# Kernel optimization log

Hardware: AMD Instinct MI355X
Metric: run time of the kernel (lower is better)

The kernel has to match this reference:

```python
import jax, jax.numpy as jnp
import numpy as np

TAU_MEM = 0.02
THRESHOLD = 0.5
RESET_POTENTIAL = 0.0
SURROGATE_BETA = 4.0
LN_EPS = 1e-6

B, T, F_IN, F_OUT = 64, 1024, 512, 512


def fast_sigmoid(x, beta):
    # Continuous fast-sigmoid surrogate spike: 0.5 * (beta*x / (1 + beta*|x|)) + 0.5
    bx = beta * x
    return 0.5 * bx / (1.0 + jnp.abs(bx)) + 0.5


def setup_inputs() -> dict:
    key = jax.random.key(0)
    k1, k2, k3 = jax.random.split(key, 3)
    spikes = jax.random.uniform(k1, (B, T, F_IN), dtype=jnp.float32)
    W = jax.random.normal(k2, (F_IN, F_OUT), dtype=jnp.float32) / np.sqrt(F_IN)
    b = jnp.zeros((F_OUT,), dtype=jnp.float32)
    ln_scale = jnp.ones((F_OUT,), dtype=jnp.float32)
    ln_bias = jnp.zeros((F_OUT,), dtype=jnp.float32)
    return {"spikes": spikes, "W": W, "b": b, "ln_scale": ln_scale, "ln_bias": ln_bias}


def reference(spikes, W, b, ln_scale, ln_bias):
    # Dense projection of input spike trains: [B,T,F_in] -> [B,T,F_out]
    currents = jnp.einsum('bti,io->bto', spikes, W) + b

    alpha = jnp.exp(jnp.float32(-1.0 / TAU_MEM))

    def lif_step(v_mem, cur):
        v_mem = alpha * v_mem + (1.0 - alpha) * cur
        spike = fast_sigmoid(v_mem - THRESHOLD, SURROGATE_BETA)
        v_mem = v_mem * (1.0 - spike) + RESET_POTENTIAL * spike
        return v_mem, spike

    v0 = jnp.zeros((spikes.shape[0], W.shape[1]), dtype=currents.dtype)
    _, out = jax.lax.scan(lif_step, v0, jnp.transpose(currents, (1, 0, 2)))  # [T,B,F]
    out = jnp.transpose(out, (1, 0, 2))  # [B,T,F]

    # LayerNorm over last axis (flax defaults: eps=1e-6, scale & bias)
    mean = jnp.mean(out, axis=-1, keepdims=True)
    var = jnp.var(out, axis=-1, keepdims=True)
    out = (out - mean) * jax.lax.rsqrt(var + LN_EPS) * ln_scale + ln_bias
    return out
```

## Files before the change

### kernel.cpp

```cpp
#include <hip/hip_runtime.h>

#define THREADS 512
#define NBLK 1024

typedef _Float16 half8 __attribute__((ext_vector_type(8)));
typedef float floatx4 __attribute__((ext_vector_type(4)));

__global__ void wcvt_kernel(const float* __restrict__ W, unsigned short* __restrict__ Wt) {
  __shared__ float tile[32][33];
  const int tx = threadIdx.x, ty = threadIdx.y;
  const int nb = blockIdx.x * 32, kb = blockIdx.y * 32;
#pragma unroll
  for (int i = 0; i < 4; ++i)
    tile[ty + 8 * i][tx] = W[(size_t)(kb + ty + 8 * i) * 512 + nb + tx];
  __syncthreads();
#pragma unroll
  for (int i = 0; i < 4; ++i) {
    union { _Float16 h; unsigned short u; } v;
    v.h = (_Float16)tile[tx][ty + 8 * i];
    Wt[(size_t)(nb + ty + 8 * i) * 512 + kb + tx] = v.u;
  }
}

#define BBASE 16384

__global__ __launch_bounds__(THREADS, 4) void lif_fused_kernel(
    const float* __restrict__ A, const unsigned short* __restrict__ Wt,
    const float* __restrict__ bias, const float* __restrict__ lnw,
    const float* __restrict__ lnb, float* __restrict__ out) {
  __shared__ uint4 smem4[5120];
  unsigned char* smem = (unsigned char*)smem4;

  const int tid  = threadIdx.x;
  const int lane = tid & 63;
  const int wave = tid >> 6;
  const int wrow = wave >> 2;
  const int wcol = wave & 3;
  const int l15  = lane & 15;
  const int g    = lane >> 4;
  const int rowBase = blockIdx.x * 64;

  const int arow  = wave * 4 + (lane >> 4);
  const int aslot = (lane & 15) ^ (arow & 15);
  const float* asrcA = A + (size_t)(rowBase + arow) * 512 + aslot * 4;
  const unsigned short* bsrcB =
      Wt + (size_t)(wave * 8 + (lane >> 3)) * 512 + ((lane & 7) ^ (lane >> 3)) * 8;

  auto stage = [&](int c) {
#pragma unroll
    for (int j = 0; j < 2; ++j) {
      int off = j * 8192 + wave * 1024;
      off = __builtin_amdgcn_readfirstlane(off);
      __builtin_amdgcn_global_load_lds(
          (const __attribute__((address_space(1))) void*)(asrcA + (size_t)j * 16384 + c * 64),
          (__attribute__((address_space(3))) void*)(smem + off), 16, 0, 0);
    }
#pragma unroll
    for (int i = 0; i < 8; ++i) {
      int off = BBASE + i * 8192 + wave * 1024;
      off = __builtin_amdgcn_readfirstlane(off);
      __builtin_amdgcn_global_load_lds(
          (const __attribute__((address_space(1))) void*)(bsrcB + (size_t)i * 32768 + c * 64),
          (__attribute__((address_space(3))) void*)(smem + off), 16, 0, 0);
    }
  };

  const int aRowB = (wrow * 32 + l15) * 256;
  const int e0 = (g * 2) ^ l15;
  const unsigned char* aP00 = smem + aRowB + e0 * 16;
  const unsigned char* aP01 = smem + aRowB + (e0 ^ 1) * 16;
  const unsigned char* aP10 = smem + aRowB + (e0 ^ 8) * 16;
  const unsigned char* aP11 = smem + aRowB + (e0 ^ 9) * 16;
  const int bRowB = BBASE + (wcol * 128 + l15) * 128;
  const int f0 = g ^ (l15 & 7);
  const unsigned char* bP0 = smem + bRowB + f0 * 16;
  const unsigned char* bP1 = smem + bRowB + (f0 ^ 4) * 16;

  floatx4 acc[2][8];
#pragma unroll
  for (int m = 0; m < 2; ++m)
#pragma unroll
    for (int n = 0; n < 8; ++n)
      acc[m][n] = (floatx4){0.f, 0.f, 0.f, 0.f};

  auto mk = [](float4 lo, float4 hi) {
    half8 t;
    t[0] = (_Float16)lo.x; t[1] = (_Float16)lo.y;
    t[2] = (_Float16)lo.z; t[3] = (_Float16)lo.w;
    t[4] = (_Float16)hi.x; t[5] = (_Float16)hi.y;
    t[6] = (_Float16)hi.z; t[7] = (_Float16)hi.w;
    return t;
  };

  auto compute = [&]() {
    {
      half8 a0 = mk(*(const float4*)aP00, *(const float4*)aP01);
      half8 a1 = mk(*(const float4*)(aP00 + 4096), *(const float4*)(aP01 + 4096));
      __builtin_amdgcn_s_setprio(1);
#pragma unroll
      for (int n = 0; n < 8; ++n) {
        half8 bf = *(const half8*)(bP0 + n * 2048);
        acc[0][n] = __builtin_amdgcn_mfma_f32_16x16x32_f16(a0, bf, acc[0][n], 0, 0, 0);
        acc[1][n] = __builtin_amdgcn_mfma_f32_16x16x32_f16(a1, bf, acc[1][n], 0, 0, 0);
      }
      __builtin_amdgcn_s_setprio(0);
    }
    {
      half8 a0 = mk(*(const float4*)aP10, *(const float4*)aP11);
      half8 a1 = mk(*(const float4*)(aP10 + 4096), *(const float4*)(aP11 + 4096));
      __builtin_amdgcn_s_setprio(1);
#pragma unroll
      for (int n = 0; n < 8; ++n) {
        half8 bf = *(const half8*)(bP1 + n * 2048);
        acc[0][n] = __builtin_amdgcn_mfma_f32_16x16x32_f16(a0, bf, acc[0][n], 0, 0, 0);
        acc[1][n] = __builtin_amdgcn_mfma_f32_16x16x32_f16(a1, bf, acc[1][n], 0, 0, 0);
      }
      __builtin_amdgcn_s_setprio(0);
    }
  };

  stage(0);
  asm volatile("s_waitcnt vmcnt(0)" ::: "memory");
  __builtin_amdgcn_s_barrier();
  __builtin_amdgcn_sched_barrier(0);

#pragma unroll 1
  for (int c = 0; c < 7; ++c) {
    compute();
    __builtin_amdgcn_sched_barrier(0);
    __builtin_amdgcn_s_barrier();
    __builtin_amdgcn_sched_barrier(0);
    stage(c + 1);
    asm volatile("s_waitcnt vmcnt(0)" ::: "memory");
    __builtin_amdgcn_s_barrier();
    __builtin_amdgcn_sched_barrier(0);
  }
  compute();
  __syncthreads();

  float bcol[8], lsc[8], lbc[8];
#pragma unroll
  for (int n = 0; n < 8; ++n) {
    const int col = wcol * 128 + n * 16 + l15;
    bcol[n] = bias[col];
    lsc[n]  = lnw[col];
    lbc[n]  = lnb[col];
  }
#pragma unroll
  for (int m = 0; m < 2; ++m)
#pragma unroll
    for (int n = 0; n < 8; ++n)
#pragma unroll
      for (int r = 0; r < 4; ++r) {
        float x  = acc[m][n][r] + bcol[n] - 0.5f;
        float bx = 4.0f * x;
        acc[m][n][r] = 0.5f * bx / (1.0f + fabsf(bx)) + 0.5f;
      }

  float rs[2][4], rq[2][4];
#pragma unroll
  for (int m = 0; m < 2; ++m)
#pragma unroll
    for (int r = 0; r < 4; ++r) {
      float s = 0.f, q = 0.f;
#pragma unroll
      for (int n = 0; n < 8; ++n) {
        float v = acc[m][n][r];
        s += v;
        q += v * v;
      }
      rs[m][r] = s;
      rq[m][r] = q;
    }
#pragma unroll
  for (int d = 1; d < 16; d <<= 1) {
#pragma unroll
    for (int m = 0; m < 2; ++m)
#pragma unroll
      for (int r = 0; r < 4; ++r) {
        rs[m][r] += __shfl_xor(rs[m][r], d, 16);
        rq[m][r] += __shfl_xor(rq[m][r], d, 16);
      }
  }

  float* redS = (float*)smem4;
  float* redQ = redS + 256;
  float* mv   = redQ + 256;
  if (l15 == 0) {
#pragma unroll
    for (int m = 0; m < 2; ++m)
#pragma unroll
      for (int r = 0; r < 4; ++r) {
        const int row = wrow * 32 + m * 16 + g * 4 + r;
        redS[row * 4 + wcol] = rs[m][r];
        redQ[row * 4 + wcol] = rq[m][r];
      }
  }
  __syncthreads();
  if (tid < 64) {
    const float S = redS[tid * 4] + redS[tid * 4 + 1] + redS[tid * 4 + 2] + redS[tid * 4 + 3];
    const float Q = redQ[tid * 4] + redQ[tid * 4 + 1] + redQ[tid * 4 + 2] + redQ[tid * 4 + 3];
    const float mean = S * (1.0f / 512.0f);
    const float var  = Q * (1.0f / 512.0f) - mean * mean;
    mv[tid * 2]     = mean;
    mv[tid * 2 + 1] = rsqrtf(var + 1e-6f);
  }
  __syncthreads();

#pragma unroll
  for (int m = 0; m < 2; ++m)
#pragma unroll
    for (int r = 0; r < 4; ++r) {
      const int row  = wrow * 32 + m * 16 + g * 4 + r;
      const float mean = mv[row * 2];
      const float rstd = mv[row * 2 + 1];
      const size_t base = (size_t)(rowBase + row) * 512;
#pragma unroll
      for (int n = 0; n < 8; ++n) {
        const int col = wcol * 128 + n * 16 + l15;
        out[base + col] = (acc[m][n][r] - mean) * rstd * lsc[n] + lbc[n];
      }
    }
}

extern "C" void kernel_launch(void* const* d_in, const int* in_sizes, int n_in,
                              void* d_out, int out_size, void* d_ws, size_t ws_size,
                              hipStream_t stream) {
  const float* spikes = (const float*)d_in[0];
  const float* W      = (const float*)d_in[1];
  const float* b      = (const float*)d_in[2];
  const float* lnw    = (const float*)d_in[3];
  const float* lnb    = (const float*)d_in[4];
  float* out = (float*)d_out;
  unsigned short* Wt = (unsigned short*)d_ws;

  wcvt_kernel<<<dim3(16, 16), dim3(32, 8), 0, stream>>>(W, Wt);
  lif_fused_kernel<<<NBLK, THREADS, 0, stream>>>(spikes, Wt, b, lnw, lnb, out);
}
```

Baseline: 91.48 us.

## Use 1024-thread blocks with triple-buffered K pipeline for the fused GEMM

Doubles the block to 1024 threads covering 128 rows, with 16 waves in an 4x4 grid, and halves the grid. The K loop is split into 16 chunks of 32 held in three LDS buffers, with global-to-LDS loads issued three chunks ahead and partial vmcnt waits. The aim is to overlap global loads with MFMA work and to load each W tile once per 128 rows instead of per 64. In exchange it uses about 147KB of LDS per block, which limits occupancy to one block per CU, and it needs one more barrier per smaller chunk.

Measured after the change: 94.80 us. 3.6% more time.

```diff
diff --git a/kernel.cpp b/kernel.cpp
--- a/kernel.cpp
+++ b/kernel.cpp
@@ -1,7 +1,8 @@
 #include <hip/hip_runtime.h>
 
-#define THREADS 512
-#define NBLK 1024
+#define THREADS 1024
+#define NBLK 512
+#define BUFSZ 49152
 
 typedef _Float16 half8 __attribute__((ext_vector_type(8)));
 typedef float floatx4 __attribute__((ext_vector_type(4)));
@@ -22,13 +23,11 @@
   }
 }
 
-#define BBASE 16384
-
 __global__ __launch_bounds__(THREADS, 4) void lif_fused_kernel(
     const float* __restrict__ A, const unsigned short* __restrict__ Wt,
     const float* __restrict__ bias, const float* __restrict__ lnw,
     const float* __restrict__ lnb, float* __restrict__ out) {
-  __shared__ uint4 smem4[5120];
+  __shared__ uint4 smem4[9216];
   unsigned char* smem = (unsigned char*)smem4;
 
   const int tid  = threadIdx.x;
@@ -38,43 +37,36 @@
   const int wcol = wave & 3;
   const int l15  = lane & 15;
   const int g    = lane >> 4;
-  const int rowBase = blockIdx.x * 64;
-
-  const int arow  = wave * 4 + (lane >> 4);
-  const int aslot = (lane & 15) ^ (arow & 15);
-  const float* asrcA = A + (size_t)(rowBase + arow) * 512 + aslot * 4;
-  const unsigned short* bsrcB =
-      Wt + (size_t)(wave * 8 + (lane >> 3)) * 512 + ((lane & 7) ^ (lane >> 3)) * 8;
-
-  auto stage = [&](int c) {
-#pragma unroll
-    for (int j = 0; j < 2; ++j) {
-      int off = j * 8192 + wave * 1024;
-      off = __builtin_amdgcn_readfirstlane(off);
-      __builtin_amdgcn_global_load_lds(
-          (const __attribute__((address_space(1))) void*)(asrcA + (size_t)j * 16384 + c * 64),
-          (__attribute__((address_space(3))) void*)(smem + off), 16, 0, 0);
-    }
-#pragma unroll
-    for (int i = 0; i < 8; ++i) {
-      int off = BBASE + i * 8192 + wave * 1024;
-      off = __builtin_amdgcn_readfirstlane(off);
-      __builtin_amdgcn_global_load_lds(
-          (const __attribute__((address_space(1))) void*)(bsrcB + (size_t)i * 32768 + c * 64),
-          (__attribute__((address_space(3))) void*)(smem + off), 16, 0, 0);
-    }
+  const int rowBase = blockIdx.x * 128;
+
+  const int arow = tid >> 3;
+  const float* asrc =
+      A + (size_t)(rowBase + arow) * 512 + ((tid & 7) ^ (arow & 7)) * 4;
+  const int brow = tid >> 2;
+  const unsigned short* bsrc =
+      Wt + (size_t)brow * 512 + ((tid & 3) ^ (brow & 3) ^ ((brow >> 2) & 3)) * 8;
+
+  auto stage = [&](int buf, int c) {
+    int offA = buf * BUFSZ + wave * 1024;
+    offA = __builtin_amdgcn_readfirstlane(offA);
+    __builtin_amdgcn_global_load_lds(
+        (const __attribute__((address_space(1))) void*)(asrc + c * 32),
+        (__attribute__((address_space(3))) void*)(smem + offA), 16, 0, 0);
+    int offB = buf * BUFSZ + 16384 + wave * 1024;
+    offB = __builtin_amdgcn_readfirstlane(offB);
+    __builtin_amdgcn_global_load_lds(
+        (const __attribute__((address_space(1))) void*)(bsrc + c * 32),
+        (__attribute__((address_space(3))) void*)(smem + offB), 16, 0, 0);
+    __builtin_amdgcn_global_load_lds(
+        (const __attribute__((address_space(1))) void*)(bsrc + 256 * 512 + c * 32),
+        (__attribute__((address_space(3))) void*)(smem + offB + 16384), 16, 0, 0);
   };
 
-  const int aRowB = (wrow * 32 + l15) * 256;
-  const int e0 = (g * 2) ^ l15;
-  const unsigned char* aP00 = smem + aRowB + e0 * 16;
-  const unsigned char* aP01 = smem + aRowB + (e0 ^ 1) * 16;
-  const unsigned char* aP10 = smem + aRowB + (e0 ^ 8) * 16;
-  const unsigned char* aP11 = smem + aRowB + (e0 ^ 9) * 16;
-  const int bRowB = BBASE + (wcol * 128 + l15) * 128;
-  const int f0 = g ^ (l15 & 7);
-  const unsigned char* bP0 = smem + bRowB + f0 * 16;
-  const unsigned char* bP1 = smem + bRowB + (f0 ^ 4) * 16;
+  const int aRB = (wrow * 32 + l15) * 128;
+  const int aO0 = (((g << 1) ^ (l15 & 7)) << 4);
+  const int aO1 = aO0 ^ 16;
+  const int bRB = 16384 + (wcol * 128 + l15) * 64 +
+                  ((g ^ (l15 & 3) ^ ((l15 >> 2) & 3)) << 4);
 
   floatx4 acc[2][8];
 #pragma unroll
@@ -92,50 +84,40 @@
     return t;
   };
 
-  auto compute = [&]() {
-    {
-      half8 a0 = mk(*(const float4*)aP00, *(const float4*)aP01);
-      half8 a1 = mk(*(const float4*)(aP00 + 4096), *(const float4*)(aP01 + 4096));
-      __builtin_amdgcn_s_setprio(1);
-#pragma unroll
-      for (int n = 0; n < 8; ++n) {
-        half8 bf = *(const half8*)(bP0 + n * 2048);
-        acc[0][n] = __builtin_amdgcn_mfma_f32_16x16x32_f16(a0, bf, acc[0][n], 0, 0, 0);
-        acc[1][n] = __builtin_amdgcn_mfma_f32_16x16x32_f16(a1, bf, acc[1][n], 0, 0, 0);
-      }
-      __builtin_amdgcn_s_setprio(0);
-    }
-    {
-      half8 a0 = mk(*(const float4*)aP10, *(const float4*)aP11);
-      half8 a1 = mk(*(const float4*)(aP10 + 4096), *(const float4*)(aP11 + 4096));
-      __builtin_amdgcn_s_setprio(1);
-#pragma unroll
-      for (int n = 0; n < 8; ++n) {
-        half8 bf = *(const half8*)(bP1 + n * 2048);
-        acc[0][n] = __builtin_amdgcn_mfma_f32_16x16x32_f16(a0, bf, acc[0][n], 0, 0, 0);
-        acc[1][n] = __builtin_amdgcn_mfma_f32_16x16x32_f16(a1, bf, acc[1][n], 0, 0, 0);
-      }
-      __builtin_amdgcn_s_setprio(0);
-    }
-  };
-
-  stage(0);
-  asm volatile("s_waitcnt vmcnt(0)" ::: "memory");
-  __builtin_amdgcn_s_barrier();
-  __builtin_amdgcn_sched_barrier(0);
-
-#pragma unroll 1
-  for (int c = 0; c < 7; ++c) {
-    compute();
+  stage(0, 0);
+  stage(1, 1);
+  stage(2, 2);
+
+#pragma unroll
+  for (int c = 0; c < 16; ++c) {
+    if (c < 14) {
+      asm volatile("s_waitcnt vmcnt(6)" ::: "memory");
+    } else if (c == 14) {
+      asm volatile("s_waitcnt vmcnt(3)" ::: "memory");
+    } else {
+      asm volatile("s_waitcnt vmcnt(0)" ::: "memory");
+    }
+    __builtin_amdgcn_s_barrier();
+    __builtin_amdgcn_sched_barrier(0);
+
+    const int buf = c % 3;
+    const unsigned char* ab = smem + buf * BUFSZ + aRB;
+    half8 a0 = mk(*(const float4*)(ab + aO0), *(const float4*)(ab + aO1));
+    half8 a1 = mk(*(const float4*)(ab + 2048 + aO0), *(const float4*)(ab + 2048 + aO1));
+    const unsigned char* bb = smem + buf * BUFSZ + bRB;
+    __builtin_amdgcn_s_setprio(1);
+#pragma unroll
+    for (int n = 0; n < 8; ++n) {
+      half8 bf = *(const half8*)(bb + n * 1024);
+      acc[0][n] = __builtin_amdgcn_mfma_f32_16x16x32_f16(a0, bf, acc[0][n], 0, 0, 0);
+      acc[1][n] = __builtin_amdgcn_mfma_f32_16x16x32_f16(a1, bf, acc[1][n], 0, 0, 0);
+    }
+    __builtin_amdgcn_s_setprio(0);
     __builtin_amdgcn_sched_barrier(0);
     __builtin_amdgcn_s_barrier();
     __builtin_amdgcn_sched_barrier(0);
-    stage(c + 1);
-    asm volatile("s_waitcnt vmcnt(0)" ::: "memory");
-    __builtin_amdgcn_s_barrier();
-    __builtin_amdgcn_sched_barrier(0);
-  }
-  compute();
+    if (c < 13) stage(buf, c + 3);
+  }
   __syncthreads();
 
   float bcol[8], lsc[8], lbc[8];
@@ -184,8 +166,8 @@
   }
 
   float* redS = (float*)smem4;
-  float* redQ = redS + 256;
-  float* mv   = redQ + 256;
+  float* redQ = redS + 512;
+  float* mv   = redQ + 512;
   if (l15 == 0) {
 #pragma unroll
     for (int m = 0; m < 2; ++m)
@@ -197,7 +179,7 @@
       }
   }
   __syncthreads();
-  if (tid < 64) {
+  if (tid < 128) {
     const float S = redS[tid * 4] + redS[tid * 4 + 1] + redS[tid * 4 + 2] + redS[tid * 4 + 3];
     const float Q = redQ[tid * 4] + redQ[tid * 4 + 1] + redQ[tid * 4 + 2] + redQ[tid * 4 + 3];
     const float mean = S * (1.0f / 512.0f);
```
